# Performance work log

Measured on AMD Instinct MI355X. Metric: run time of the kernel, lower is better.

Reference implementation:

```python
import jax, jax.numpy as jnp
import numpy as np

B, H, S, DK = 4, 16, 2048, 64


def setup_inputs() -> dict:
    key = jax.random.key(0)
    kq, kk, kv, km = jax.random.split(key, 4)
    Q = jax.random.normal(kq, (B, H, S, DK), dtype=jnp.float32)
    K = jax.random.normal(kk, (B, H, S, DK), dtype=jnp.float32)
    V = jax.random.normal(kv, (B, H, S, DK), dtype=jnp.float32)
    mask = (jax.random.uniform(km, (B, 1, S, S)) > 0.1).astype(jnp.float32)
    return {"Q": Q, "K": K, "V": V, "mask": mask}


def reference(Q, K, V, mask):
    d_k = Q.shape[-1]
    # unnormalized exp scores (no max subtraction), multiplicative mask
    scores = jnp.exp(jnp.einsum("bhqd,bhkd->bhqk", Q, K) / jnp.sqrt(jnp.float32(d_k)))
    scores = scores * mask
    attn = scores / (jnp.sum(scores, axis=-1, keepdims=True) + 1e-8)
    return jnp.einsum("bhqk,bhkd->bhqd", attn, V)
```

## Files before the change

### kernel.cpp

```cpp
#include <hip/hip_runtime.h>

namespace {
constexpr int S  = 2048;
constexpr int D  = 64;
constexpr int BQ = 256;
constexpr int BK = 64;
constexpr int NT = 512;
constexpr int NKT = S / BK;

typedef short bf16x8 __attribute__((ext_vector_type(8)));
typedef float f32x4  __attribute__((ext_vector_type(4)));

__device__ inline unsigned short bf16c(float x) {
  __bf16 h = (__bf16)x;
  return __builtin_bit_cast(unsigned short, h);
}
__device__ inline unsigned pk2(float a, float b) {
  return (unsigned)bf16c(a) | ((unsigned)bf16c(b) << 16);
}
__device__ inline void gld_lds16(const void* g, void* l) {
  __builtin_amdgcn_global_load_lds(
      (const __attribute__((address_space(1))) unsigned int*)g,
      (__attribute__((address_space(3))) unsigned int*)l, 16, 0, 0);
}
#if __has_builtin(__builtin_amdgcn_exp2f)
__device__ inline float exp2v(float x) { return __builtin_amdgcn_exp2f(x); }
#else
__device__ inline float exp2v(float x) { return __expf(x * 0.6931471805599453f); }
#endif

__device__ inline int kswz_of_row(int row) {
  return (row & 3) | (((row >> 3) & 1) << 2);
}

__device__ inline bf16x8 mk_pa(f32x4 s0, f32x4 s1, unsigned mw0, unsigned mw1) {
  uint4 u;
  u.x = pk2(exp2v(s0[0]), exp2v(s0[1])) & __builtin_amdgcn_perm(0u, mw0, 0x01010000u);
  u.y = pk2(exp2v(s0[2]), exp2v(s0[3])) & __builtin_amdgcn_perm(0u, mw0, 0x03030202u);
  u.z = pk2(exp2v(s1[0]), exp2v(s1[1])) & __builtin_amdgcn_perm(0u, mw1, 0x01010000u);
  u.w = pk2(exp2v(s1[2]), exp2v(s1[3])) & __builtin_amdgcn_perm(0u, mw1, 0x03030202u);
  return __builtin_bit_cast(bf16x8, u);
}

__global__ __launch_bounds__(256) void prep_k(const float* __restrict__ K,
                                              unsigned short* __restrict__ Kws) {
  int gid = blockIdx.x * 256 + threadIdx.x;
  int row = gid >> 3;
  int g   = gid & 7;
  const float* src = K + (size_t)row * 64 + g * 8;
  float4 a = *(const float4*)src;
  float4 b = *(const float4*)(src + 4);
  uint4 w;
  w.x = pk2(a.x, a.y); w.y = pk2(a.z, a.w);
  w.z = pk2(b.x, b.y); w.w = pk2(b.z, b.w);
  *(uint4*)(Kws + (size_t)row * 64 + ((g ^ kswz_of_row(row)) * 8)) = w;
}

__global__ __launch_bounds__(512) void prep_v(const float* __restrict__ V,
                                              unsigned short* __restrict__ Vws) {
  __shared__ __align__(16) unsigned char smem[51200];
  const int t    = threadIdx.x;
  const int half = t >> 8;
  const int tsub = t & 255;
  const size_t tile = (size_t)blockIdx.x * 2 + half;
  float* tl = (float*)smem + half * (64 * 68);
  unsigned short* so = (unsigned short*)(smem + 34816) + half * 4096;
  const float* src = V + tile * (64 * 64);
#pragma unroll
  for (int rep = 0; rep < 4; ++rep) {
    int idx = tsub + rep * 256;
    int row = idx >> 4, d4 = idx & 15;
    float4 v = *(const float4*)(src + row * 64 + d4 * 4);
    *(float4*)(tl + row * 68 + d4 * 4) = v;
  }
  __syncthreads();
#pragma unroll
  for (int rep = 0; rep < 2; ++rep) {
    int d  = (tsub & 31) + rep * 32;
    int kg = tsub >> 5;
    float x[8];
#pragma unroll
    for (int j = 0; j < 8; ++j) x[j] = tl[(kg * 8 + j) * 68 + d];
    uint4 w;
    w.x = pk2(x[0], x[1]); w.y = pk2(x[2], x[3]);
    w.z = pk2(x[4], x[5]); w.w = pk2(x[6], x[7]);
    *(uint4*)(so + d * 64 + ((kg ^ (d & 7)) * 8)) = w;
  }
  __syncthreads();
  unsigned short* dstT = Vws + tile * (64 * 64);
#pragma unroll
  for (int rep = 0; rep < 2; ++rep) {
    int i = tsub + rep * 256;
    *(uint4*)(dstT + i * 8) = *(const uint4*)(so + i * 8);
  }
}

__global__ __launch_bounds__(512) void prep_m(const float* __restrict__ M,
                                              unsigned char* __restrict__ M2) {
  __shared__ unsigned nibs[32][129];
  const int t  = threadIdx.x;
  const int b  = blockIdx.x >> 6;
  const int qg = blockIdx.x & 63;
  const float* src = M + ((size_t)b * S + (size_t)qg * 32) * S;
#pragma unroll
  for (int pass = 0; pass < 8; ++pass) {
    int idx = pass * 512 + t;
    int q  = idx >> 7;
    int kc = idx & 127;
    const float* p = src + (size_t)q * S + kc * 16;
    unsigned w = 0;
#pragma unroll
    for (int j = 0; j < 4; ++j) {
      float4 v = *(const float4*)(p + j * 4);
      unsigned nib = (v.x != 0.f ? 1u : 0u) | (v.y != 0.f ? 2u : 0u) |
                     (v.z != 0.f ? 4u : 0u) | (v.w != 0.f ? 8u : 0u);
      w |= nib << (8 * j);
    }
    nibs[q][kc] = w;
  }
  __syncthreads();
  const int e    = t & 127;
  const int lane = e >> 1, g = e & 1;
  const int n16  = lane & 15, quad = lane >> 4;
  const int qq   = g * 16 + n16;
  const int c    = quad >> 1;
  const int sh0  = 8 * ((2 * quad) & 3);
  unsigned char* dstb = M2 + ((size_t)b * NKT * 64 + qg) * 2048 + (size_t)e * 16;
#pragma unroll
  for (int i = 0; i < 8; ++i) {
    int kt = (t >> 7) + i * 4;
    unsigned d0 = nibs[qq][kt * 4 + c];
    unsigned d1 = nibs[qq][kt * 4 + 2 + c];
    unsigned n00 = (d0 >> sh0) & 0xFu;
    unsigned n01 = (d0 >> (sh0 + 8)) & 0xFu;
    unsigned n10 = (d1 >> sh0) & 0xFu;
    unsigned n11 = (d1 >> (sh0 + 8)) & 0xFu;
    uint4 out;
    out.x = ((n00 * 0x00204081u) & 0x01010101u) * 255u;
    out.y = ((n01 * 0x00204081u) & 0x01010101u) * 255u;
    out.z = ((n10 * 0x00204081u) & 0x01010101u) * 255u;
    out.w = ((n11 * 0x00204081u) & 0x01010101u) * 255u;
    *(uint4*)(dstb + (size_t)kt * (64 * 64 * 32)) = out;
  }
}

__global__ __launch_bounds__(NT, 4)
void attn3(const float* __restrict__ Qg, const unsigned char* __restrict__ M2,
           const unsigned short* __restrict__ Kws,
           const unsigned short* __restrict__ Vws,
           float* __restrict__ Og) {
  __shared__ __align__(16) unsigned short sK[2][BK * D];
  __shared__ __align__(16) unsigned short sV[2][BK * D];

  const int t    = threadIdx.x;
  const int wave = t >> 6;
  const int lane = t & 63;
  const int quad = lane >> 4;
  const int n16  = lane & 15;

  const int bh = blockIdx.y;
  const int b  = bh >> 4;
  const int q0 = blockIdx.x * BQ;
  const int qg = blockIdx.x * 8 + wave;

  const unsigned short* Kb = Kws + (size_t)bh * S * D;
  const unsigned short* Vb = Vws + (size_t)bh * S * D;
  const unsigned char* Mp = M2 + (((size_t)b * NKT * 64 + qg) * 64 + lane) * 32;
  constexpr size_t MKT = (size_t)64 * 64 * 32;

  const int h2 = n16 >> 2, rr = n16 & 3;
  const int krow0 = (8 * h2 + rr) * 64;

  const int sw = n16 & 7;
  const int ga = (quad ^ sw) * 8;
  const int gb = ((quad + 4) ^ sw) * 8;

  constexpr float QS = 0.18033688011112042f;
  const float* QbA = Qg + ((size_t)bh * S + q0 + wave * 32 + n16) * D;
  bf16x8 aqA[2], aqB[2];
#pragma unroll
  for (int ks = 0; ks < 2; ++ks) {
    const float* qp = QbA + ks * 32 + quad * 8;
    float4 x = *(const float4*)qp;
    float4 y = *(const float4*)(qp + 4);
    bf16x8 a;
    a[0] = (short)bf16c(x.x * QS); a[1] = (short)bf16c(x.y * QS);
    a[2] = (short)bf16c(x.z * QS); a[3] = (short)bf16c(x.w * QS);
    a[4] = (short)bf16c(y.x * QS); a[5] = (short)bf16c(y.y * QS);
    a[6] = (short)bf16c(y.z * QS); a[7] = (short)bf16c(y.w * QS);
    aqA[ks] = a;
    const float* qp2 = qp + 16 * D;
    float4 x2 = *(const float4*)qp2;
    float4 y2 = *(const float4*)(qp2 + 4);
    bf16x8 a2;
    a2[0] = (short)bf16c(x2.x * QS); a2[1] = (short)bf16c(x2.y * QS);
    a2[2] = (short)bf16c(x2.z * QS); a2[3] = (short)bf16c(x2.w * QS);
    a2[4] = (short)bf16c(y2.x * QS); a2[5] = (short)bf16c(y2.y * QS);
    a2[6] = (short)bf16c(y2.z * QS); a2[7] = (short)bf16c(y2.w * QS);
    aqB[ks] = a2;
  }

  bf16x8 ones;
#pragma unroll
  for (int i = 0; i < 8; ++i) ones[i] = (short)0x3F80;

  f32x4 oA[4], oB[4];
#pragma unroll
  for (int nt = 0; nt < 4; ++nt) {
    oA[nt] = (f32x4){0.f, 0.f, 0.f, 0.f};
    oB[nt] = (f32x4){0.f, 0.f, 0.f, 0.f};
  }
  f32x4 rsA = (f32x4){0.f, 0.f, 0.f, 0.f};
  f32x4 rsB = (f32x4){0.f, 0.f, 0.f, 0.f};

  gld_lds16(Kb + wave * 512 + lane * 8, &sK[0][wave * 512]);
  gld_lds16(Vb + wave * 512 + lane * 8, &sV[0][wave * 512]);
  uint4 mkA[2], mkB[2];
  mkA[0] = *(const uint4*)Mp;
  mkB[0] = *(const uint4*)(Mp + 16);

#pragma unroll 2
  for (int kt = 0; kt < NKT; ++kt) {
    const int cur = kt & 1, nxt = cur ^ 1;
    __syncthreads();

    if (kt + 1 < NKT) {
      gld_lds16(Kb + (size_t)(kt + 1) * (BK * D) + wave * 512 + lane * 8,
                &sK[nxt][wave * 512]);
      gld_lds16(Vb + (size_t)(kt + 1) * (BK * D) + wave * 512 + lane * 8,
                &sV[nxt][wave * 512]);
      mkA[nxt] = *(const uint4*)(Mp + (size_t)(kt + 1) * MKT);
      mkB[nxt] = *(const uint4*)(Mp + (size_t)(kt + 1) * MKT + 16);
    }

    bf16x8 paA[2], paB[2];
#pragma unroll
    for (int ks = 0; ks < 2; ++ks) {
      const unsigned short* base = &sK[cur][krow0 + ks * 2048];
      bf16x8 k0a = *(const bf16x8*)(base + ga);
      bf16x8 k0b = *(const bf16x8*)(base + gb);
      bf16x8 k1a = *(const bf16x8*)(base + 256 + ga);
      bf16x8 k1b = *(const bf16x8*)(base + 256 + gb);
      const f32x4 z = (f32x4){0.f, 0.f, 0.f, 0.f};

      f32x4 sA0 = __builtin_amdgcn_mfma_f32_16x16x32_bf16(k0a, aqA[0], z, 0, 0, 0);
      sA0 = __builtin_amdgcn_mfma_f32_16x16x32_bf16(k0b, aqA[1], sA0, 0, 0, 0);
      f32x4 sA1 = __builtin_amdgcn_mfma_f32_16x16x32_bf16(k1a, aqA[0], z, 0, 0, 0);
      sA1 = __builtin_amdgcn_mfma_f32_16x16x32_bf16(k1b, aqA[1], sA1, 0, 0, 0);
      paA[ks] = mk_pa(sA0, sA1, ks ? mkA[cur].z : mkA[cur].x,
                                ks ? mkA[cur].w : mkA[cur].y);

      f32x4 sB0 = __builtin_amdgcn_mfma_f32_16x16x32_bf16(k0a, aqB[0], z, 0, 0, 0);
      sB0 = __builtin_amdgcn_mfma_f32_16x16x32_bf16(k0b, aqB[1], sB0, 0, 0, 0);
      f32x4 sB1 = __builtin_amdgcn_mfma_f32_16x16x32_bf16(k1a, aqB[0], z, 0, 0, 0);
      sB1 = __builtin_amdgcn_mfma_f32_16x16x32_bf16(k1b, aqB[1], sB1, 0, 0, 0);
      paB[ks] = mk_pa(sB0, sB1, ks ? mkB[cur].z : mkB[cur].x,
                                ks ? mkB[cur].w : mkB[cur].y);
    }

    rsA = __builtin_amdgcn_mfma_f32_16x16x32_bf16(ones, paA[0], rsA, 0, 0, 0);
    rsA = __builtin_amdgcn_mfma_f32_16x16x32_bf16(ones, paA[1], rsA, 0, 0, 0);
    rsB = __builtin_amdgcn_mfma_f32_16x16x32_bf16(ones, paB[0], rsB, 0, 0, 0);
    rsB = __builtin_amdgcn_mfma_f32_16x16x32_bf16(ones, paB[1], rsB, 0, 0, 0);

#pragma unroll
    for (int nt = 0; nt < 4; ++nt) {
      const int row = nt * 16 + n16;
      bf16x8 v0 = *(const bf16x8*)(sV[cur] + row * 64 + ga);
      bf16x8 v1 = *(const bf16x8*)(sV[cur] + row * 64 + gb);
      oA[nt] = __builtin_amdgcn_mfma_f32_16x16x32_bf16(v0, paA[0], oA[nt], 0, 0, 0);
      oA[nt] = __builtin_amdgcn_mfma_f32_16x16x32_bf16(v1, paA[1], oA[nt], 0, 0, 0);
      oB[nt] = __builtin_amdgcn_mfma_f32_16x16x32_bf16(v0, paB[0], oB[nt], 0, 0, 0);
      oB[nt] = __builtin_amdgcn_mfma_f32_16x16x32_bf16(v1, paB[1], oB[nt], 0, 0, 0);
    }
  }

  const float invA = 1.0f / (rsA[0] + 1e-8f);
  const float invB = 1.0f / (rsB[0] + 1e-8f);
  float* OA = Og + ((size_t)bh * S + q0 + wave * 32 + n16) * D;
#pragma unroll
  for (int nt = 0; nt < 4; ++nt) {
    float4 wa = make_float4(oA[nt][0] * invA, oA[nt][1] * invA,
                            oA[nt][2] * invA, oA[nt][3] * invA);
    *(float4*)(OA + nt * 16 + quad * 4) = wa;
    float4 wb = make_float4(oB[nt][0] * invB, oB[nt][1] * invB,
                            oB[nt][2] * invB, oB[nt][3] * invB);
    *(float4*)(OA + 16 * D + nt * 16 + quad * 4) = wb;
  }
}
}

extern "C" void kernel_launch(void* const* d_in, const int* in_sizes, int n_in,
                              void* d_out, int out_size, void* d_ws, size_t ws_size,
                              hipStream_t stream) {
  const float* Q = (const float*)d_in[0];
  const float* K = (const float*)d_in[1];
  const float* V = (const float*)d_in[2];
  const float* M = (const float*)d_in[3];
  float* O = (float*)d_out;

  unsigned short* Kws = (unsigned short*)d_ws;
  unsigned short* Vws = Kws + (size_t)64 * S * D;
  unsigned char*  M2  = (unsigned char*)(Vws + (size_t)64 * S * D);

  prep_k<<<dim3(64 * S * D / 8 / 256), 256, 0, stream>>>(K, Kws);
  prep_v<<<dim3(64 * NKT / 2), 512, 0, stream>>>(V, Vws);
  prep_m<<<dim3(4 * 64), 512, 0, stream>>>(M, M2);
  attn3<<<dim3(S / BQ, 64), NT, 0, stream>>>(Q, M2, Kws, Vws, O);
}
```

Baseline: 268.6 us.

## Software-pipeline PV MFMA one tile behind QK and softmax

Restructures the key loop so the P·V accumulation for tile kt-1 is issued before the QK^T and mask/exp work for tile kt. The goal is to interleave independent MFMA chains with the exp/convert VALU work and hide latency. The V shared buffer grows to four stages so the previous tile's V stays resident, and the unroll factor rises to 4. This costs extra LDS per block, which may lower occupancy, and extra registers to carry the previous P fragments.

```diff
diff --git a/kernel.cpp b/kernel.cpp
--- a/kernel.cpp
+++ b/kernel.cpp
@@ -150,7 +150,7 @@
            const unsigned short* __restrict__ Vws,
            float* __restrict__ Og) {
   __shared__ __align__(16) unsigned short sK[2][BK * D];
-  __shared__ __align__(16) unsigned short sV[2][BK * D];
+  __shared__ __align__(16) unsigned short sV[4][BK * D];
 
   const int t    = threadIdx.x;
   const int wave = t >> 6;
@@ -213,30 +213,44 @@
   f32x4 rsA = (f32x4){0.f, 0.f, 0.f, 0.f};
   f32x4 rsB = (f32x4){0.f, 0.f, 0.f, 0.f};
 
+  bf16x8 paPA[2], paPB[2];
+
   gld_lds16(Kb + wave * 512 + lane * 8, &sK[0][wave * 512]);
   gld_lds16(Vb + wave * 512 + lane * 8, &sV[0][wave * 512]);
   uint4 mkA[2], mkB[2];
   mkA[0] = *(const uint4*)Mp;
   mkB[0] = *(const uint4*)(Mp + 16);
 
-#pragma unroll 2
+#pragma unroll 4
   for (int kt = 0; kt < NKT; ++kt) {
-    const int cur = kt & 1, nxt = cur ^ 1;
     __syncthreads();
 
     if (kt + 1 < NKT) {
-      gld_lds16(Kb + (size_t)(kt + 1) * (BK * D) + wave * 512 + lane * 8,
-                &sK[nxt][wave * 512]);
-      gld_lds16(Vb + (size_t)(kt + 1) * (BK * D) + wave * 512 + lane * 8,
-                &sV[nxt][wave * 512]);
-      mkA[nxt] = *(const uint4*)(Mp + (size_t)(kt + 1) * MKT);
-      mkB[nxt] = *(const uint4*)(Mp + (size_t)(kt + 1) * MKT + 16);
-    }
-
-    bf16x8 paA[2], paB[2];
+      const size_t gbase = (size_t)(kt + 1) * (BK * D);
+      gld_lds16(Kb + gbase + wave * 512 + lane * 8, &sK[(kt + 1) & 1][wave * 512]);
+      gld_lds16(Vb + gbase + wave * 512 + lane * 8, &sV[(kt + 1) & 3][wave * 512]);
+      mkA[(kt + 1) & 1] = *(const uint4*)(Mp + (size_t)(kt + 1) * MKT);
+      mkB[(kt + 1) & 1] = *(const uint4*)(Mp + (size_t)(kt + 1) * MKT + 16);
+    }
+
+    if (kt > 0) {
+      const unsigned short* sVp = sV[(kt - 1) & 3];
+#pragma unroll
+      for (int nt = 0; nt < 4; ++nt) {
+        const int row = nt * 16 + n16;
+        bf16x8 v0 = *(const bf16x8*)(sVp + row * 64 + ga);
+        bf16x8 v1 = *(const bf16x8*)(sVp + row * 64 + gb);
+        oA[nt] = __builtin_amdgcn_mfma_f32_16x16x32_bf16(v0, paPA[0], oA[nt], 0, 0, 0);
+        oA[nt] = __builtin_amdgcn_mfma_f32_16x16x32_bf16(v1, paPA[1], oA[nt], 0, 0, 0);
+        oB[nt] = __builtin_amdgcn_mfma_f32_16x16x32_bf16(v0, paPB[0], oB[nt], 0, 0, 0);
+        oB[nt] = __builtin_amdgcn_mfma_f32_16x16x32_bf16(v1, paPB[1], oB[nt], 0, 0, 0);
+      }
+    }
+
+    bf16x8 paCA[2], paCB[2];
 #pragma unroll
     for (int ks = 0; ks < 2; ++ks) {
-      const unsigned short* base = &sK[cur][krow0 + ks * 2048];
+      const unsigned short* base = &sK[kt & 1][krow0 + ks * 2048];
       bf16x8 k0a = *(const bf16x8*)(base + ga);
       bf16x8 k0b = *(const bf16x8*)(base + gb);
       bf16x8 k1a = *(const bf16x8*)(base + 256 + ga);
@@ -247,31 +261,37 @@
       sA0 = __builtin_amdgcn_mfma_f32_16x16x32_bf16(k0b, aqA[1], sA0, 0, 0, 0);
       f32x4 sA1 = __builtin_amdgcn_mfma_f32_16x16x32_bf16(k1a, aqA[0], z, 0, 0, 0);
       sA1 = __builtin_amdgcn_mfma_f32_16x16x32_bf16(k1b, aqA[1], sA1, 0, 0, 0);
-      paA[ks] = mk_pa(sA0, sA1, ks ? mkA[cur].z : mkA[cur].x,
-                                ks ? mkA[cur].w : mkA[cur].y);
+      paCA[ks] = mk_pa(sA0, sA1, ks ? mkA[kt & 1].z : mkA[kt & 1].x,
+                                 ks ? mkA[kt & 1].w : mkA[kt & 1].y);
 
       f32x4 sB0 = __builtin_amdgcn_mfma_f32_16x16x32_bf16(k0a, aqB[0], z, 0, 0, 0);
       sB0 = __builtin_amdgcn_mfma_f32_16x16x32_bf16(k0b, aqB[1], sB0, 0, 0, 0);
       f32x4 sB1 = __builtin_amdgcn_mfma_f32_16x16x32_bf16(k1a, aqB[0], z, 0, 0, 0);
       sB1 = __builtin_amdgcn_mfma_f32_16x16x32_bf16(k1b, aqB[1], sB1, 0, 0, 0);
-      paB[ks] = mk_pa(sB0, sB1, ks ? mkB[cur].z : mkB[cur].x,
-                                ks ? mkB[cur].w : mkB[cur].y);
-    }
-
-    rsA = __builtin_amdgcn_mfma_f32_16x16x32_bf16(ones, paA[0], rsA, 0, 0, 0);
-    rsA = __builtin_amdgcn_mfma_f32_16x16x32_bf16(ones, paA[1], rsA, 0, 0, 0);
-    rsB = __builtin_amdgcn_mfma_f32_16x16x32_bf16(ones, paB[0], rsB, 0, 0, 0);
-    rsB = __builtin_amdgcn_mfma_f32_16x16x32_bf16(ones, paB[1], rsB, 0, 0, 0);
-
+      paCB[ks] = mk_pa(sB0, sB1, ks ? mkB[kt & 1].z : mkB[kt & 1].x,
+                                 ks ? mkB[kt & 1].w : mkB[kt & 1].y);
+    }
+
+    rsA = __builtin_amdgcn_mfma_f32_16x16x32_bf16(ones, paCA[0], rsA, 0, 0, 0);
+    rsA = __builtin_amdgcn_mfma_f32_16x16x32_bf16(ones, paCA[1], rsA, 0, 0, 0);
+    rsB = __builtin_amdgcn_mfma_f32_16x16x32_bf16(ones, paCB[0], rsB, 0, 0, 0);
+    rsB = __builtin_amdgcn_mfma_f32_16x16x32_bf16(ones, paCB[1], rsB, 0, 0, 0);
+
+    paPA[0] = paCA[0]; paPA[1] = paCA[1];
+    paPB[0] = paCB[0]; paPB[1] = paCB[1];
+  }
+
+  {
+    const unsigned short* sVp = sV[(NKT - 1) & 3];
 #pragma unroll
     for (int nt = 0; nt < 4; ++nt) {
       const int row = nt * 16 + n16;
-      bf16x8 v0 = *(const bf16x8*)(sV[cur] + row * 64 + ga);
-      bf16x8 v1 = *(const bf16x8*)(sV[cur] + row * 64 + gb);
-      oA[nt] = __builtin_amdgcn_mfma_f32_16x16x32_bf16(v0, paA[0], oA[nt], 0, 0, 0);
-      oA[nt] = __builtin_amdgcn_mfma_f32_16x16x32_bf16(v1, paA[1], oA[nt], 0, 0, 0);
-      oB[nt] = __builtin_amdgcn_mfma_f32_16x16x32_bf16(v0, paB[0], oB[nt], 0, 0, 0);
-      oB[nt] = __builtin_amdgcn_mfma_f32_16x16x32_bf16(v1, paB[1], oB[nt], 0, 0, 0);
+      bf16x8 v0 = *(const bf16x8*)(sVp + row * 64 + ga);
+      bf16x8 v1 = *(const bf16x8*)(sVp + row * 64 + gb);
+      oA[nt] = __builtin_amdgcn_mfma_f32_16x16x32_bf16(v0, paPA[0], oA[nt], 0, 0, 0);
+      oA[nt] = __builtin_amdgcn_mfma_f32_16x16x32_bf16(v1, paPA[1], oA[nt], 0, 0, 0);
+      oB[nt] = __builtin_amdgcn_mfma_f32_16x16x32_bf16(v0, paPB[0], oB[nt], 0, 0, 0);
+      oB[nt] = __builtin_amdgcn_mfma_f32_16x16x32_bf16(v1, paPB[1], oB[nt], 0, 0, 0);
     }
   }
 
```

Result: slower. 274.8 us (+2.3%).
